# Optimization experiments

Measured on AMD Instinct MI355X. Metric: run time of the kernel, lower is better.

## Reference

```python
import math
import jax, jax.numpy as jnp
import numpy as np

C, H, W, N = 128, 64, 64, 32


def setup_inputs() -> dict:
    key = jax.random.key(0)
    k = jax.random.split(key, 6)
    std = 0.02
    return {
        "x": jax.random.normal(k[0], (N, C, H, W), dtype=jnp.float32),
        # p_3: 1x1 conv, weight [out=C, in=3C]
        "w3": jax.random.normal(k[1], (C, 3 * C), dtype=jnp.float32) * std,
        "p5_w": jax.random.normal(k[2], (1, 1, H, W), dtype=jnp.float32) * std,
        # p_6: conv (3,1), dilation (3,1), weight [O=C, I=C, 3, 1]
        "w6": jax.random.normal(k[3], (C, C, 3, 1), dtype=jnp.float32) * std,
        "p8_w": jax.random.normal(k[4], (1, C, 1, 1), dtype=jnp.float32) * std,
        "p12_w": jax.random.normal(k[5], (1, 1, 3, H, 1), dtype=jnp.float32) * std,
    }


def reference(x, w3, p5_w, w6, p8_w, p12_w):
    n, c, h, w = x.shape
    # F.unfold(x, (1,3), dilation=(1,2), padding=(0,2)) -> taps at w-2, w, w+2 (zero padded)
    xp = jnp.pad(x, ((0, 0), (0, 0), (0, 0), (2, 2)))
    t1 = jnp.stack([xp[..., 0:w], xp[..., 2:w + 2], xp[..., 4:w + 4]], axis=2)  # [n,c,3,h,w]
    t2 = t1.max(axis=2)                                                          # [n,c,h,w]
    # p_3: 1x1 conv over 3c channels
    t3 = jnp.einsum('nkhw,ok->nohw', t1.reshape(n, c * 3, h, w), w3)            # [n,c,h,w]
    t4 = jnp.maximum(t3[:, :, None], t1)                                         # [n,c,3,h,w]
    t5 = p5_w * t2
    # p_6: (3,1) conv, dilation (3,1), padding (3,0) -> same spatial size
    t6 = jax.lax.conv_general_dilated(
        t5, w6, window_strides=(1, 1), padding=((3, 3), (0, 0)),
        rhs_dilation=(3, 1), dimension_numbers=('NCHW', 'OIHW', 'NCHW'))         # [n,c,h,w]
    t7 = jnp.maximum(x, t6)
    t8 = p8_w * t7
    # bmm: [n,c,hw] x [n,hw,3c] -> [n,c,3c]
    t9 = jnp.einsum('ncp,nkp->nck', t8.reshape(n, c, h * w),
                    t1.reshape(n, c * 3, h * w)) / math.sqrt(h * w)
    t10 = t7[:, :, None] + t4                                                    # [n,c,3,h,w]
    t11 = jnp.maximum(t6[:, :, None], t10)                                       # [n,c,3,h,w]
    t12 = p12_w * t11
    # bmm: [n,hw,3c] x [n,3c,c] -> [n,hw,c]
    t13 = jnp.einsum('nkp,nck->npc', t12.reshape(n, c * 3, h * w), t9) / math.sqrt(c * 3)
    return t13.reshape(n, h, w, c).transpose(0, 3, 1, 2)                         # [n,c,h,w]
```

## Files before the change

kernel.cpp:

```cpp
#include <hip/hip_runtime.h>

#define C_   128
#define P_   4096
#define K3   384
#define CP   (C_*P_)
#define NB_  32

typedef __attribute__((ext_vector_type(8))) short short8;
typedef __attribute__((ext_vector_type(4))) short short4v;
typedef __attribute__((ext_vector_type(4))) float f32x4;

__device__ __forceinline__ short f2bf(float f) {
  union { float f; unsigned u; } v; v.f = f;
  unsigned r = v.u + 0x7fffu + ((v.u >> 16) & 1u);
  return (short)(r >> 16);
}
__device__ __forceinline__ float bf2f(short b) {
  union { unsigned u; float f; } v; v.u = ((unsigned)(unsigned short)b) << 16;
  return v.f;
}
__device__ __forceinline__ void gl_lds16(const void* g, void* l) {
  __builtin_amdgcn_global_load_lds(
      (const __attribute__((address_space(1))) unsigned int*)g,
      (__attribute__((address_space(3))) unsigned int*)l, 16, 0, 0);
}

__global__ __launch_bounds__(256) void prep_kernel(const float* __restrict__ w3,
                                                   const float* __restrict__ w6,
                                                   short* __restrict__ w3p,
                                                   short* __restrict__ w6p) {
  int idx = blockIdx.x * 256 + threadIdx.x;
  int m = idx / K3, kp = idx - m * K3;
  int j = kp >> 7, c = kp & 127;
  w3p[idx] = f2bf(w3[m * K3 + c * 3 + j]);
  w6p[idx] = f2bf(w6[m * K3 + c * 3 + j]);
}

__global__ __launch_bounds__(256) void xk_kernel(const float* __restrict__ x,
                                                 short* __restrict__ xb,
                                                 short* __restrict__ xT) {
  int b = blockIdx.x;
  int pt = b & 63, ct = (b >> 6) & 1, n = b >> 7;
  int p0 = pt * 64, c0 = ct * 64;
  const float* xn = x + (size_t)n * CP;
  short* xbn = xb + (size_t)n * CP;
  short* xTn = xT + (size_t)n * CP;
  __shared__ short Ls[64][68];
  int tid = threadIdx.x;
#pragma unroll
  for (int it = 0; it < 4; ++it) {
    int fid = tid + it * 256;
    int i = fid >> 4, j4 = fid & 15;
    f32x4 v = *(const f32x4*)(xn + (c0 + i) * P_ + p0 + j4 * 4);
    short4v s;
#pragma unroll
    for (int r = 0; r < 4; ++r) s[r] = f2bf(v[r]);
    *(short4v*)(xbn + (c0 + i) * P_ + p0 + j4 * 4) = s;
    *(short4v*)(&Ls[i][j4 * 4]) = s;
  }
  __syncthreads();
#pragma unroll
  for (int it = 0; it < 4; ++it) {
    int oid = tid + it * 256;
    int pr = oid >> 4, cg = oid & 15, cb = cg * 4;
    short4v a;
#pragma unroll
    for (int r = 0; r < 4; ++r) a[r] = Ls[cb + r][pr];
    *(short4v*)(xTn + (p0 + pr) * C_ + c0 + cb) = a;
  }
}

__global__ __launch_bounds__(256, 4) void g12_kernel(const short* __restrict__ w3p,
                                                     const short* __restrict__ w6p,
                                                     const float* __restrict__ p5,
                                                     const short* __restrict__ xT,
                                                     short* __restrict__ t3T,
                                                     short* __restrict__ t6T,
                                                     short* __restrict__ t7T) {
  int blk = blockIdx.x;
  int role = blk & 1;
  int b = blk >> 1;
  int n = b >> 5, pt = b & 31, p0 = pt * 128;
  int tid = threadIdx.x, lane = tid & 63, wv = tid >> 6;
  int wm = (wv & 1) * 64, wp = (wv >> 1) * 64;
  const short* Ap = role ? w3p : w6p;
  const short* xTn = xT + (size_t)n * CP;
  __shared__ __align__(16) short As[2][4][128][8];
  __shared__ __align__(16) short Bs[2][4][128][8];
  f32x4 acc[4][4] = {};
  short8 bm[2], bl[2], br[2];
  float bp5[2];

  auto stageA = [&](int ks, int bf) {
    int k0 = (ks % 3) * 128 + (ks / 3) * 32;
#pragma unroll
    for (int it = 0; it < 2; ++it) {
      int slot = tid + it * 256;
      int q = slot >> 7, m = slot & 127;
      gl_lds16(Ap + m * K3 + k0 + q * 8, &As[bf][q][m][0]);
    }
  };
  auto loadB = [&](int ks) {
    int jr = ks % 3;
#pragma unroll
    for (int it = 0; it < 2; ++it) {
      int slot = tid + it * 256;
      int q = slot & 3, pc = slot >> 2;
      int p = p0 + pc;
      int c0k = (ks / 3) * 32 + q * 8;
      if (role) {
        int d = 2 * (jr - 1);
        int prc = min(max(p + d, 0), P_ - 1);
        bm[it] = *(const short8*)(xTn + (size_t)prc * C_ + c0k);
      } else {
        int pr = p + 192 * (jr - 1);
        int prc = min(max(pr, 0), P_ - 1);
        int w2 = prc & 63;
        const short* rb = xTn + (size_t)prc * C_ + c0k;
        short8 zero = {};
        bm[it] = *(const short8*)rb;
        bl[it] = (w2 >= 2) ? *(const short8*)(rb - 2 * C_) : zero;
        br[it] = (w2 < 62) ? *(const short8*)(rb + 2 * C_) : zero;
        bp5[it] = p5[prc];
      }
    }
  };
  auto writeB = [&](int ks, int bf) {
    int jr = ks % 3;
#pragma unroll
    for (int it = 0; it < 2; ++it) {
      int slot = tid + it * 256;
      int q = slot & 3, pc = slot >> 2;
      int p = p0 + pc;
      short8 zero = {};
      short8 v;
      if (role) {
        int d = 2 * (jr - 1);
        int wd = (p & 63) + d;
        v = bm[it];
        if (!(wd >= 0 && wd < 64)) v = zero;
      } else {
        int pr = p + 192 * (jr - 1);
        bool rv = (pr >= 0 && pr < P_);
#pragma unroll
        for (int jj = 0; jj < 8; ++jj)
          v[jj] = f2bf(bp5[it] * fmaxf(fmaxf(bf2f(bl[it][jj]), bf2f(bm[it][jj])), bf2f(br[it][jj])));
        if (!rv) v = zero;
      }
      *(short8*)(&Bs[bf][q][pc][0]) = v;
    }
  };

  stageA(0, 0);
  loadB(0);
  writeB(0, 0);
  __syncthreads();
#pragma unroll 2
  for (int ks = 0; ks < 12; ++ks) {
    int cur = ks & 1, nxt = cur ^ 1;
    if (ks < 11) { stageA(ks + 1, nxt); loadB(ks + 1); }
    int row = lane & 15, q = lane >> 4;
    short8 a[4], bb[4];
#pragma unroll
    for (int im = 0; im < 4; ++im) a[im] = *(const short8*)(&As[cur][q][wm + im * 16 + row][0]);
#pragma unroll
    for (int ip = 0; ip < 4; ++ip) bb[ip] = *(const short8*)(&Bs[cur][q][wp + ip * 16 + row][0]);
#pragma unroll
    for (int im = 0; im < 4; ++im)
#pragma unroll
      for (int ip = 0; ip < 4; ++ip)
        acc[im][ip] = __builtin_amdgcn_mfma_f32_16x16x32_bf16(a[im], bb[ip], acc[im][ip], 0, 0, 0);
    if (ks < 11) writeB(ks + 1, nxt);
    __syncthreads();
  }
  int col = lane & 15, rq = lane >> 4;
  if (role) {
    short* t3Tn = t3T + (size_t)n * CP;
#pragma unroll
    for (int im = 0; im < 4; ++im)
#pragma unroll
      for (int ip = 0; ip < 4; ++ip) {
        int m0 = wm + im * 16 + rq * 4;
        int p = p0 + wp + ip * 16 + col;
        short4v s;
#pragma unroll
        for (int r = 0; r < 4; ++r) s[r] = f2bf(acc[im][ip][r]);
        *(short4v*)(t3Tn + (size_t)p * C_ + m0) = s;
      }
  } else {
    short* t6Tn = t6T + (size_t)n * CP;
    short* t7Tn = t7T + (size_t)n * CP;
#pragma unroll
    for (int im = 0; im < 4; ++im)
#pragma unroll
      for (int ip = 0; ip < 4; ++ip) {
        int m0 = wm + im * 16 + rq * 4;
        int p = p0 + wp + ip * 16 + col;
        short4v ax = *(const short4v*)(xTn + (size_t)p * C_ + m0);
        short4v s6, s7;
#pragma unroll
        for (int r = 0; r < 4; ++r) {
          float t6v = acc[im][ip][r];
          float t7v = fmaxf(bf2f(ax[r]), t6v);
          s6[r] = f2bf(t6v);
          s7[r] = f2bf(t7v);
        }
        *(short4v*)(t6Tn + (size_t)p * C_ + m0) = s6;
        *(short4v*)(t7Tn + (size_t)p * C_ + m0) = s7;
      }
  }
}

__global__ __launch_bounds__(256, 4) void g3_kernel(const short* __restrict__ xb,
                                                    const short* __restrict__ t7T,
                                                    float* __restrict__ t9) {
  int blk = blockIdx.x;
  int nb = blk % 3;
  int tmp = blk / 3;
  int n = tmp & 31, sk = tmp >> 5;
  int d = 2 * (nb - 1);
  int tid = threadIdx.x, lane = tid & 63, wv = tid >> 6;
  int wm = (wv & 1) * 64, wp = (wv >> 1) * 64;
  const short* xbn = xb + (size_t)n * CP;
  const short* t7n = t7T + (size_t)n * CP;
  __shared__ __align__(16) short As[2][4][128][8];
  __shared__ __align__(16) short Bs[2][4][128][8];
  f32x4 acc[4][4] = {};
  short8 av[2], bv[2];

  auto loadAB = [&](int ks) {
    int pp0 = sk * 512 + ks * 32;
#pragma unroll
    for (int it = 0; it < 2; ++it) {
      int slot = tid + it * 256;
      int q = slot >> 7, rr = slot & 127;
      int pb = pp0 + q * 8;
      const int* src = (const int*)(xbn + rr * P_ + pb + d);
      union { int i[4]; short8 s; } u;
#pragma unroll
      for (int t = 0; t < 4; ++t) u.i[t] = src[t];
      av[it] = u.s;
      const short* bp = t7n + (size_t)pb * C_ + rr;
      short8 w;
#pragma unroll
      for (int j = 0; j < 8; ++j) w[j] = bp[j * C_];
      bv[it] = w;
    }
  };
  auto writeAB = [&](int ks, int bf) {
    int pp0 = sk * 512 + ks * 32;
#pragma unroll
    for (int it = 0; it < 2; ++it) {
      int slot = tid + it * 256;
      int q = slot >> 7, rr = slot & 127;
      int pb = pp0 + q * 8;
      short8 v = av[it];
      int w0 = pb & 63;
      if (nb == 0) { if (w0 == 0) { v[0] = 0; v[1] = 0; } }
      else if (nb == 2) { if (w0 == 56) { v[6] = 0; v[7] = 0; } }
      *(short8*)(&As[bf][q][rr][0]) = v;
      *(short8*)(&Bs[bf][q][rr][0]) = bv[it];
    }
  };

  loadAB(0);
  writeAB(0, 0);
  __syncthreads();
#pragma unroll 2
  for (int ks = 0; ks < 16; ++ks) {
    int cur = ks & 1, nxt = cur ^ 1;
    if (ks < 15) loadAB(ks + 1);
    int row = lane & 15, q = lane >> 4;
    short8 a[4], bb[4];
#pragma unroll
    for (int im = 0; im < 4; ++im) a[im] = *(const short8*)(&As[cur][q][wm + im * 16 + row][0]);
#pragma unroll
    for (int ip = 0; ip < 4; ++ip) bb[ip] = *(const short8*)(&Bs[cur][q][wp + ip * 16 + row][0]);
#pragma unroll
    for (int im = 0; im < 4; ++im)
#pragma unroll
      for (int ip = 0; ip < 4; ++ip)
        acc[im][ip] = __builtin_amdgcn_mfma_f32_16x16x32_bf16(a[im], bb[ip], acc[im][ip], 0, 0, 0);
    if (ks < 15) writeAB(ks + 1, nxt);
    __syncthreads();
  }
  int col = lane & 15, rq = lane >> 4;
  float* t9n = t9 + (size_t)n * (K3 * C_);
#pragma unroll
  for (int im = 0; im < 4; ++im)
#pragma unroll
    for (int ip = 0; ip < 4; ++ip)
#pragma unroll
      for (int r = 0; r < 4; ++r) {
        int kp = nb * 128 + wm + im * 16 + rq * 4 + r;
        int c = wp + ip * 16 + col;
        atomicAdd(&t9n[(size_t)kp * C_ + c], acc[im][ip][r]);
      }
}

__global__ __launch_bounds__(256) void t9s_kernel(const float* __restrict__ t9,
                                                  const float* __restrict__ p8,
                                                  short* __restrict__ t9b) {
  int b = blockIdx.x;
  int n = b / 6, kt = b - n * 6;
  int k0 = kt * 64;
  const float INV = 1.0f / (64.0f * 19.5959179423f);
  const float* t9n = t9 + (size_t)n * (K3 * C_);
  short* t9bn = t9b + (size_t)n * (C_ * K3);
  __shared__ float L[64][132];
  int tid = threadIdx.x;
#pragma unroll
  for (int it = 0; it < 8; ++it) {
    int s = tid + it * 256;
    int k = s >> 5, c4 = s & 31;
    f32x4 v = *(const f32x4*)(t9n + (size_t)(k0 + k) * C_ + c4 * 4);
    *(f32x4*)(&L[k][c4 * 4]) = v;
  }
  __syncthreads();
#pragma unroll
  for (int it = 0; it < 2; ++it) {
    int s = tid + it * 256;
    int c = s >> 2, kg = s & 3;
    float sc = p8[c] * INV;
    short8 o0, o1;
#pragma unroll
    for (int j = 0; j < 8; ++j) o0[j] = f2bf(L[kg * 16 + j][c] * sc);
#pragma unroll
    for (int j = 0; j < 8; ++j) o1[j] = f2bf(L[kg * 16 + 8 + j][c] * sc);
    short* op = t9bn + (size_t)c * K3 + k0 + kg * 16;
    *(short8*)(op) = o0;
    *(short8*)(op + 8) = o1;
  }
}

__global__ __launch_bounds__(256, 4) void g4_kernel(const short* __restrict__ t9b,
                                                    const float* __restrict__ p12,
                                                    const short* __restrict__ t3T,
                                                    const short* __restrict__ t6T,
                                                    const short* __restrict__ t7T,
                                                    const short* __restrict__ xT,
                                                    float* __restrict__ out) {
  int b = blockIdx.x;
  int n = b >> 5, pt = b & 31, p0 = pt * 128;
  int tid = threadIdx.x, lane = tid & 63, wv = tid >> 6;
  int wm = (wv & 1) * 64, wp = (wv >> 1) * 64;
  const short* t9n = t9b + (size_t)n * (K3 * C_);
  const short* t3n = t3T + (size_t)n * CP;
  const short* t6n = t6T + (size_t)n * CP;
  const short* t7n = t7T + (size_t)n * CP;
  const short* xTn = xT + (size_t)n * CP;
  __shared__ __align__(16) short As[2][4][128][8];
  __shared__ __align__(16) short Bs[2][4][128][8];
  f32x4 acc[4][4] = {};
  short8 r6[2], r7[2], r3[2], rx[2];

  auto stageA = [&](int ks, int bf) {
    int k0 = (ks % 3) * 128 + (ks / 3) * 32;
#pragma unroll
    for (int it = 0; it < 2; ++it) {
      int slot = tid + it * 256;
      int q = slot >> 7, m = slot & 127;
      gl_lds16(t9n + (size_t)m * K3 + k0 + q * 8, &As[bf][q][m][0]);
    }
  };
  auto loadB = [&](int ks) {
    int j = ks % 3, d = 2 * (j - 1);
    int k0c = (ks / 3) * 32;
#pragma unroll
    for (int it = 0; it < 2; ++it) {
      int slot = tid + it * 256;
      int q = slot & 3, pc = slot >> 2;
      int p = p0 + pc;
      int c0k = k0c + q * 8;
      size_t base = (size_t)p * C_ + c0k;
      r6[it] = *(const short8*)(t6n + base);
      r7[it] = *(const short8*)(t7n + base);
      r3[it] = *(const short8*)(t3n + base);
      int pr = min(max(p + d, 0), P_ - 1);
      rx[it] = *(const short8*)(xTn + (size_t)pr * C_ + c0k);
    }
  };
  auto writeB = [&](int ks, int bf) {
    int j = ks % 3, d = 2 * (j - 1);
#pragma unroll
    for (int it = 0; it < 2; ++it) {
      int slot = tid + it * 256;
      int q = slot & 3, pc = slot >> 2;
      int p = p0 + pc;
      float s12 = p12[j * 64 + (p >> 6)];
      int wd = (p & 63) + d;
      bool valid = (wd >= 0 && wd < 64);
      short8 zero = {};
      short8 ax = rx[it];
      if (!valid) ax = zero;
      short8 v;
#pragma unroll
      for (int jj = 0; jj < 8; ++jj) {
        float t11 = fmaxf(bf2f(r6[it][jj]), bf2f(r7[it][jj]) + fmaxf(bf2f(r3[it][jj]), bf2f(ax[jj])));
        v[jj] = f2bf(s12 * t11);
      }
      *(short8*)(&Bs[bf][q][pc][0]) = v;
    }
  };

  stageA(0, 0);
  loadB(0);
  writeB(0, 0);
  __syncthreads();
#pragma unroll 2
  for (int ks = 0; ks < 12; ++ks) {
    int cur = ks & 1, nxt = cur ^ 1;
    if (ks < 11) { stageA(ks + 1, nxt); loadB(ks + 1); }
    int row = lane & 15, q = lane >> 4;
    short8 a[4], bb[4];
#pragma unroll
    for (int im = 0; im < 4; ++im) a[im] = *(const short8*)(&As[cur][q][wm + im * 16 + row][0]);
#pragma unroll
    for (int ip = 0; ip < 4; ++ip) bb[ip] = *(const short8*)(&Bs[cur][q][wp + ip * 16 + row][0]);
#pragma unroll
    for (int im = 0; im < 4; ++im)
#pragma unroll
      for (int ip = 0; ip < 4; ++ip)
        acc[im][ip] = __builtin_amdgcn_mfma_f32_16x16x32_bf16(a[im], bb[ip], acc[im][ip], 0, 0, 0);
    if (ks < 11) writeB(ks + 1, nxt);
    __syncthreads();
  }
  int col = lane & 15, rq = lane >> 4;
#pragma unroll
  for (int im = 0; im < 4; ++im)
#pragma unroll
    for (int ip = 0; ip < 4; ++ip)
#pragma unroll
      for (int r = 0; r < 4; ++r) {
        int m = wm + im * 16 + rq * 4 + r;
        int p = p0 + wp + ip * 16 + col;
        out[(size_t)n * CP + m * P_ + p] = acc[im][ip][r];
      }
}

extern "C" void kernel_launch(void* const* d_in, const int* in_sizes, int n_in,
                              void* d_out, int out_size, void* d_ws, size_t ws_size,
                              hipStream_t stream) {
  const float* x   = (const float*)d_in[0];
  const float* w3  = (const float*)d_in[1];
  const float* p5  = (const float*)d_in[2];
  const float* w6  = (const float*)d_in[3];
  const float* p8  = (const float*)d_in[4];
  const float* p12 = (const float*)d_in[5];
  float* out = (float*)d_out;

  char* ws = (char*)d_ws;
  const size_t RB = (size_t)NB_ * CP * 2;
  size_t off = 256;
  short* xb  = (short*)(ws + off); off += RB;
  short* xT  = (short*)(ws + off); off += RB;
  short* t3T = (short*)(ws + off); off += RB;
  short* t6T = (short*)(ws + off); off += RB;
  short* t7T = (short*)(ws + off); off += RB;
  float* t9  = (float*)(ws + off); off += (size_t)NB_ * K3 * C_ * 4;
  short* w3p = (short*)(ws + off); off += 49152 * 2;
  short* w6p = (short*)(ws + off); off += 49152 * 2;
  short* t9b = xb;

  prep_kernel<<<192, 256, 0, stream>>>(w3, w6, w3p, w6p);
  xk_kernel<<<4096, 256, 0, stream>>>(x, xb, xT);
  g12_kernel<<<2048, 256, 0, stream>>>(w3p, w6p, p5, xT, t3T, t6T, t7T);
  hipMemsetAsync(t9, 0, (size_t)NB_ * K3 * C_ * sizeof(float), stream);
  g3_kernel<<<768, 256, 0, stream>>>(xb, t7T, t9);
  t9s_kernel<<<192, 256, 0, stream>>>(t9, p8, t9b);
  g4_kernel<<<1024, 256, 0, stream>>>(t9b, p12, t3T, t6T, t7T, xT, out);
}
```

Before: 462.4 us.

## Precompute t12 operand in a separate kernel and stage it via direct LDS loads

Moves the elementwise t11/t12 computation out of the final GEMM's operand-load path into a new standalone kernel. That kernel writes the three shifted-tap variants in place over the t3T/t6T/t7T buffers, which sit next to each other in the workspace. The GEMM then loads its B operand with asynchronous global-to-LDS copies, like its A operand, which removes register staging and VALU work from its main loop. The cost is an extra full pass over several large bf16 buffers (four reads and three writes) plus one more kernel launch.

```diff
diff --git a/kernel.cpp b/kernel.cpp
--- a/kernel.cpp
+++ b/kernel.cpp
@@ -333,26 +333,58 @@
   }
 }
 
+__global__ __launch_bounds__(256) void t12k_kernel(const float* __restrict__ p12,
+                                                   const short* __restrict__ xT,
+                                                   short* __restrict__ t3T,
+                                                   short* __restrict__ t6T,
+                                                   short* __restrict__ t7T) {
+  int idx = blockIdx.x * 256 + threadIdx.x;
+  int cg = idx & 15;
+  int p  = (idx >> 4) & 4095;
+  int n  = idx >> 16;
+  size_t base = (size_t)n * CP + (size_t)p * C_ + cg * 8;
+  short8 a3 = *(const short8*)(t3T + base);
+  short8 a6 = *(const short8*)(t6T + base);
+  short8 a7 = *(const short8*)(t7T + base);
+  const short* xn = xT + (size_t)n * CP;
+  int c0 = cg * 8;
+  int h = p >> 6, w = p & 63;
+  short8 outv[3];
+#pragma unroll
+  for (int j = 0; j < 3; ++j) {
+    int d = 2 * (j - 1);
+    int wd = w + d;
+    bool valid = (wd >= 0 && wd < 64);
+    int pr = min(max(p + d, 0), P_ - 1);
+    short8 ax = *(const short8*)(xn + (size_t)pr * C_ + c0);
+    short8 zero = {};
+    if (!valid) ax = zero;
+    float s12 = p12[j * 64 + h];
+    short8 v;
+#pragma unroll
+    for (int jj = 0; jj < 8; ++jj) {
+      float t11 = fmaxf(bf2f(a6[jj]), bf2f(a7[jj]) + fmaxf(bf2f(a3[jj]), bf2f(ax[jj])));
+      v[jj] = f2bf(s12 * t11);
+    }
+    outv[j] = v;
+  }
+  *(short8*)(t3T + base) = outv[0];
+  *(short8*)(t6T + base) = outv[1];
+  *(short8*)(t7T + base) = outv[2];
+}
+
 __global__ __launch_bounds__(256, 4) void g4_kernel(const short* __restrict__ t9b,
-                                                    const float* __restrict__ p12,
-                                                    const short* __restrict__ t3T,
-                                                    const short* __restrict__ t6T,
-                                                    const short* __restrict__ t7T,
-                                                    const short* __restrict__ xT,
+                                                    const short* __restrict__ t12,
                                                     float* __restrict__ out) {
   int b = blockIdx.x;
   int n = b >> 5, pt = b & 31, p0 = pt * 128;
   int tid = threadIdx.x, lane = tid & 63, wv = tid >> 6;
   int wm = (wv & 1) * 64, wp = (wv >> 1) * 64;
   const short* t9n = t9b + (size_t)n * (K3 * C_);
-  const short* t3n = t3T + (size_t)n * CP;
-  const short* t6n = t6T + (size_t)n * CP;
-  const short* t7n = t7T + (size_t)n * CP;
-  const short* xTn = xT + (size_t)n * CP;
+  const size_t SL = (size_t)NB_ * CP;
   __shared__ __align__(16) short As[2][4][128][8];
   __shared__ __align__(16) short Bs[2][4][128][8];
   f32x4 acc[4][4] = {};
-  short8 r6[2], r7[2], r3[2], rx[2];
 
   auto stageA = [&](int ks, int bf) {
     int k0 = (ks % 3) * 128 + (ks / 3) * 32;
@@ -363,54 +395,24 @@
       gl_lds16(t9n + (size_t)m * K3 + k0 + q * 8, &As[bf][q][m][0]);
     }
   };
-  auto loadB = [&](int ks) {
-    int j = ks % 3, d = 2 * (j - 1);
-    int k0c = (ks / 3) * 32;
-#pragma unroll
-    for (int it = 0; it < 2; ++it) {
-      int slot = tid + it * 256;
-      int q = slot & 3, pc = slot >> 2;
-      int p = p0 + pc;
-      int c0k = k0c + q * 8;
-      size_t base = (size_t)p * C_ + c0k;
-      r6[it] = *(const short8*)(t6n + base);
-      r7[it] = *(const short8*)(t7n + base);
-      r3[it] = *(const short8*)(t3n + base);
-      int pr = min(max(p + d, 0), P_ - 1);
-      rx[it] = *(const short8*)(xTn + (size_t)pr * C_ + c0k);
-    }
-  };
-  auto writeB = [&](int ks, int bf) {
-    int j = ks % 3, d = 2 * (j - 1);
-#pragma unroll
-    for (int it = 0; it < 2; ++it) {
-      int slot = tid + it * 256;
-      int q = slot & 3, pc = slot >> 2;
-      int p = p0 + pc;
-      float s12 = p12[j * 64 + (p >> 6)];
-      int wd = (p & 63) + d;
-      bool valid = (wd >= 0 && wd < 64);
-      short8 zero = {};
-      short8 ax = rx[it];
-      if (!valid) ax = zero;
-      short8 v;
-#pragma unroll
-      for (int jj = 0; jj < 8; ++jj) {
-        float t11 = fmaxf(bf2f(r6[it][jj]), bf2f(r7[it][jj]) + fmaxf(bf2f(r3[it][jj]), bf2f(ax[jj])));
-        v[jj] = f2bf(s12 * t11);
-      }
-      *(short8*)(&Bs[bf][q][pc][0]) = v;
+  auto stageB = [&](int ks, int bf) {
+    int j = ks % 3, cb = ks / 3;
+    const short* src = t12 + (size_t)j * SL + (size_t)n * CP;
+#pragma unroll
+    for (int it = 0; it < 2; ++it) {
+      int slot = tid + it * 256;
+      int q = slot >> 7, pc = slot & 127;
+      gl_lds16(src + (size_t)(p0 + pc) * C_ + cb * 32 + q * 8, &Bs[bf][q][pc][0]);
     }
   };
 
   stageA(0, 0);
-  loadB(0);
-  writeB(0, 0);
+  stageB(0, 0);
   __syncthreads();
 #pragma unroll 2
   for (int ks = 0; ks < 12; ++ks) {
     int cur = ks & 1, nxt = cur ^ 1;
-    if (ks < 11) { stageA(ks + 1, nxt); loadB(ks + 1); }
+    if (ks < 11) { stageA(ks + 1, nxt); stageB(ks + 1, nxt); }
     int row = lane & 15, q = lane >> 4;
     short8 a[4], bb[4];
 #pragma unroll
@@ -422,7 +424,6 @@
 #pragma unroll
       for (int ip = 0; ip < 4; ++ip)
         acc[im][ip] = __builtin_amdgcn_mfma_f32_16x16x32_bf16(a[im], bb[ip], acc[im][ip], 0, 0, 0);
-    if (ks < 11) writeB(ks + 1, nxt);
     __syncthreads();
   }
   int col = lane & 15, rq = lane >> 4;
@@ -468,5 +469,6 @@
   hipMemsetAsync(t9, 0, (size_t)NB_ * K3 * C_ * sizeof(float), stream);
   g3_kernel<<<768, 256, 0, stream>>>(xb, t7T, t9);
   t9s_kernel<<<192, 256, 0, stream>>>(t9, p8, t9b);
-  g4_kernel<<<1024, 256, 0, stream>>>(t9b, p12, t3T, t6T, t7T, xT, out);
-}
+  t12k_kernel<<<8192, 256, 0, stream>>>(p12, xT, t3T, t6T, t7T);
+  g4_kernel<<<1024, 256, 0, stream>>>(t9b, t3T, out);
+}
```

New measurement: 399.8 us. -13.5%, faster.
